# Optimization experiments

Measured on AMD Instinct MI355X. Metric: run time of the kernel, lower is better.

Reference implementation:

```python
import jax, jax.numpy as jnp
import numpy as np

COST_CLASS, COST_MASK, COST_DICE = 2.0, 5.0, 5.0
NUM_POINTS = 12544

def setup_inputs() -> dict:
    key = jax.random.key(0)
    k1, k2, k3, k4, k5 = jax.random.split(key, 5)
    bs, Q, K = 4, 100, 134
    H = W = 256
    M = 80
    P = H * W
    pred_logits = jax.random.normal(k1, (bs, Q, K), dtype=jnp.float32)
    pred_masks = jax.random.normal(k2, (bs, Q, H, W), dtype=jnp.float32)
    tgt_labels = jax.random.randint(k3, (M,), 0, K - 1, dtype=jnp.int32)
    # binary target masks, stored as float (matches .float() in torch code)
    tgt_masks = (jax.random.uniform(k4, (M, H, W)) > 0.5).astype(jnp.float32)
    # random subset of points without replacement (torch.randperm[:num_points])
    point_idx = jax.random.permutation(k5, P)[:NUM_POINTS].astype(jnp.int32)
    return {"pred_logits": pred_logits, "pred_masks": pred_masks,
            "tgt_labels": tgt_labels, "tgt_masks": tgt_masks,
            "point_idx": point_idx}

def reference(pred_logits, pred_masks, tgt_labels, tgt_masks, point_idx):
    bs, Q, K = pred_logits.shape
    N = bs * Q
    M = tgt_masks.shape[0]
    Pn = point_idx.shape[0]

    # class cost: -p[n, tgt_id[m]]
    out_prob = jax.nn.softmax(pred_logits.reshape(N, K), axis=-1)
    tgt_ids = jnp.clip(tgt_labels.astype(jnp.int32), 0, K - 1)
    cost_class = -out_prob[:, tgt_ids]                      # (N, M)

    # sampled mask logits / targets
    x = pred_masks.reshape(N, -1)[:, point_idx]             # (N, Pn) logits
    y = tgt_masks.reshape(M, -1)[:, point_idx]              # (M, Pn) binary float

    # BCE-with-logits cost, separable form:
    # mean_p[softplus(x) - x*y] = mean_p softplus(x) - (x @ y^T)/Pn
    sp_mean = jnp.mean(jax.nn.softplus(x), axis=-1)         # (N,)
    xy = jnp.einsum('np,mp->nm', x, y)                      # (N, M)
    cost_mask = sp_mean[:, None] - xy / Pn

    # dice cost
    s = jax.nn.sigmoid(x)                                   # (N, Pn)
    numer = 2.0 * jnp.einsum('np,mp->nm', s, y)             # (N, M)
    denom = jnp.sum(s, axis=-1)[:, None] + jnp.sum(y, axis=-1)[None, :]
    cost_dice = 1.0 - (numer + 1.0) / (denom + 1.0)

    C = COST_CLASS * cost_class + COST_MASK * cost_mask + COST_DICE * cost_dice
    return C.reshape(bs, Q, M)
```

## Files before the change

### kernel.cpp

```cpp
#include <hip/hip_runtime.h>
#include <math.h>

#define N_ROWS 400
#define M_ROWS 80
#define K_CLS  134
#define PN     12544
#define PFULL  65536
#define WORDS  (PFULL / 32)
#define TSTEPS 392
#define NSUB   25
#define KCG    49
#define TPB    2
#define NM     (N_ROWS * M_ROWS)
#define CHUNK  16384
#define CPB    (PFULL / CHUNK)

typedef __attribute__((ext_vector_type(4))) float  f32x4;
typedef __attribute__((ext_vector_type(8))) __bf16 bf16x8;

__device__ __forceinline__ float wave_reduce_sum(float v) {
#pragma unroll
    for (int off = 32; off > 0; off >>= 1) v += __shfl_down(v, off, 64);
    return v;
}

__global__ __launch_bounds__(1024) void sort_softmax_kernel(
        const int* __restrict__ point_idx,
        unsigned int* __restrict__ bitmap_g, int* __restrict__ rank_g,
        float* __restrict__ rowS_acc, float* __restrict__ rowSP_acc,
        float* __restrict__ ysum_acc,
        const float* __restrict__ pred_logits,
        float* __restrict__ rowmax, float* __restrict__ rowsum) {
    int tid = threadIdx.x;
    if (blockIdx.x == 0) {
        __shared__ unsigned int bits[WORDS];
        __shared__ int wtot[16], wbase[16];
        bits[tid] = 0u; bits[tid + 1024] = 0u;
        if (tid < N_ROWS) { rowS_acc[tid] = 0.f; rowSP_acc[tid] = 0.f; }
        if (tid < M_ROWS) ysum_acc[tid] = 0.f;
        __syncthreads();
        for (int i = tid; i < PN; i += 1024) {
            int p = point_idx[i];
            atomicOr(&bits[p >> 5], 1u << (p & 31));
        }
        __syncthreads();
        unsigned int w0 = bits[tid * 2], w1 = bits[tid * 2 + 1];
        int cnt = __popc(w0) + __popc(w1);
        int lane = tid & 63, wid = tid >> 6;
        int v = cnt;
#pragma unroll
        for (int off = 1; off < 64; off <<= 1) {
            int u = __shfl_up(v, off, 64);
            if (lane >= off) v += u;
        }
        if (lane == 63) wtot[wid] = v;
        __syncthreads();
        if (tid == 0) {
            int run = 0;
#pragma unroll
            for (int i = 0; i < 16; ++i) { wbase[i] = run; run += wtot[i]; }
        }
        __syncthreads();
        int base = wbase[wid] + (v - cnt);
        bitmap_g[tid * 2]     = w0;
        bitmap_g[tid * 2 + 1] = w1;
        rank_g[tid * 2]       = base;
        rank_g[tid * 2 + 1]   = base + __popc(w0);
    } else {
        int wave = tid >> 6, lane = tid & 63;
        int n = (blockIdx.x - 1) * 16 + wave;
        const float* row = pred_logits + n * K_CLS;
        float mx = -1e30f;
        for (int k = lane; k < K_CLS; k += 64) mx = fmaxf(mx, row[k]);
#pragma unroll
        for (int off = 32; off > 0; off >>= 1) mx = fmaxf(mx, __shfl_down(mx, off, 64));
        mx = __shfl(mx, 0, 64);
        float se = 0.f;
        for (int k = lane; k < K_CLS; k += 64) se += expf(row[k] - mx);
        se = wave_reduce_sum(se);
        if (lane == 0) { rowmax[n] = mx; rowsum[n] = se; }
    }
}

__global__ __launch_bounds__(256) void compact_kernel(
        const float* __restrict__ pred_masks, const float* __restrict__ tgt_masks,
        const unsigned int* __restrict__ bitmap_g, const int* __restrict__ rank_g,
        __bf16* __restrict__ Xc, __bf16* __restrict__ Sc, __bf16* __restrict__ Yb,
        float* __restrict__ rowS_acc, float* __restrict__ rowSP_acc,
        float* __restrict__ ysum_acc) {
    __shared__ unsigned int sb[CHUNK / 32];
    __shared__ int swb[CHUNK / 32];
    __shared__ float aS[4], aSP[4];
    int b   = blockIdx.x;
    int row = b / CPB, ch = b % CPB;
    int tid = threadIdx.x;
    int wave = tid >> 6, lane = tid & 63;
    int w0  = ch * (CHUNK / 32);
    sb[tid]        = bitmap_g[w0 + tid];
    sb[tid + 256]  = bitmap_g[w0 + tid + 256];
    swb[tid]       = rank_g[w0 + tid];
    swb[tid + 256] = rank_g[w0 + tid + 256];
    __syncthreads();
    int p0 = ch * CHUNK;

    if (row < N_ROWS) {
        const float* src = pred_masks + (size_t)row * PFULL + p0;
        __bf16* xrow = Xc + (size_t)row * PN;
        __bf16* srow = Sc + (size_t)row * PN;
        float sS = 0.f, sSP = 0.f;
#pragma unroll
        for (int it = 0; it < CHUNK / (256 * 4); ++it) {
            int e = (it * 256 + tid) * 4;
            f32x4 v = *(const f32x4*)(src + e);
            unsigned int w = sb[e >> 5];
            int r = swb[e >> 5] + __popc(w & ((1u << (e & 31)) - 1u));
            unsigned int m4 = (w >> (e & 31)) & 0xFu;
            if (m4) {
#pragma unroll
                for (int k = 0; k < 4; ++k) if (m4 & (1u << k)) {
                    float x  = v[k];
                    float ax = fabsf(x);
                    float ee = __expf(-ax);
                    float den = 1.f + ee;
                    float inv = __builtin_amdgcn_rcpf(den);
                    float sig = (x >= 0.f) ? inv : ee * inv;
                    float sp  = fmaxf(x, 0.f) + __logf(den);
                    xrow[r] = (__bf16)x;
                    srow[r] = (__bf16)sig;
                    sS += sig; sSP += sp; ++r;
                }
            }
        }
        sS  = wave_reduce_sum(sS);
        sSP = wave_reduce_sum(sSP);
        if (lane == 0) { aS[wave] = sS; aSP[wave] = sSP; }
        __syncthreads();
        if (tid == 0)
            atomicAdd(&rowS_acc[row], aS[0] + aS[1] + aS[2] + aS[3]);
        else if (tid == 1)
            atomicAdd(&rowSP_acc[row], aSP[0] + aSP[1] + aSP[2] + aSP[3]);
    } else {
        int m = row - N_ROWS;
        const float* src = tgt_masks + (size_t)m * PFULL + p0;
        int j = m >> 4, colL = m & 15;
        float ys = 0.f;
#pragma unroll
        for (int it = 0; it < CHUNK / (256 * 4); ++it) {
            int e = (it * 256 + tid) * 4;
            f32x4 v = *(const f32x4*)(src + e);
            unsigned int w = sb[e >> 5];
            int r = swb[e >> 5] + __popc(w & ((1u << (e & 31)) - 1u));
            unsigned int m4 = (w >> (e & 31)) & 0xFu;
            if (m4) {
#pragma unroll
                for (int k = 0; k < 4; ++k) if (m4 & (1u << k)) {
                    float y = (v[k] > 0.5f) ? 1.f : 0.f;
                    int t = r >> 5, rr = r & 31;
                    int quad = rr >> 3, jj = rr & 7;
                    Yb[(((size_t)t * 5 + j) * 64 + quad * 16 + colL) * 8 + jj]
                        = (__bf16)y;
                    ys += y; ++r;
                }
            }
        }
        ys = wave_reduce_sum(ys);
        if (lane == 0) aS[wave] = ys;
        __syncthreads();
        if (tid == 0)
            atomicAdd(&ysum_acc[m], aS[0] + aS[1] + aS[2] + aS[3]);
    }
}

__global__ __launch_bounds__(256) void gemm_kernel(
        const __bf16* __restrict__ Xc, const __bf16* __restrict__ Sc,
        const __bf16* __restrict__ Yb,
        float* __restrict__ xypart, float* __restrict__ sypart) {
    __shared__ float red[4][20][64];
    int tid = threadIdx.x;
    int wave = tid >> 6, lane = tid & 63;
    int colL = lane & 15, quad = lane >> 4;
    int nsub = blockIdx.x % NSUB, kcg = blockIdx.x / NSUB;
    int n0 = nsub * 16;
    int tbase = kcg * (TPB * 4) + wave * TPB;
    const bf16x8* Yf = (const bf16x8*)Yb;

    f32x4 accX[5], accS[5];
    f32x4 zero = {0.f, 0.f, 0.f, 0.f};
#pragma unroll
    for (int j = 0; j < 5; ++j) { accX[j] = zero; accS[j] = zero; }

    bf16x8 aX[TPB], aS[TPB], Bb[TPB][5];
#pragma unroll
    for (int i = 0; i < TPB; ++i) {
        int t = tbase + i;
        size_t aoff = (size_t)(n0 + colL) * PN + t * 32 + quad * 8;
        aX[i] = *(const bf16x8*)(Xc + aoff);
        aS[i] = *(const bf16x8*)(Sc + aoff);
        const bf16x8* q = Yf + (size_t)(t * 5) * 64 + lane;
#pragma unroll
        for (int j = 0; j < 5; ++j) Bb[i][j] = q[(size_t)j * 64];
    }
#pragma unroll
    for (int i = 0; i < TPB; ++i) {
#pragma unroll
        for (int j = 0; j < 5; ++j) {
            accX[j] = __builtin_amdgcn_mfma_f32_16x16x32_bf16(aX[i], Bb[i][j], accX[j], 0, 0, 0);
            accS[j] = __builtin_amdgcn_mfma_f32_16x16x32_bf16(aS[i], Bb[i][j], accS[j], 0, 0, 0);
        }
    }

#pragma unroll
    for (int j = 0; j < 5; ++j)
#pragma unroll
        for (int r = 0; r < 4; ++r) red[wave][j * 4 + r][lane] = accX[j][r];
    __syncthreads();
#pragma unroll
    for (int v0 = 0; v0 < 5; ++v0) {
        int v = wave * 5 + v0;
        float s = red[0][v][lane] + red[1][v][lane] + red[2][v][lane] + red[3][v][lane];
        int j = v >> 2, r = v & 3;
        int n = n0 + quad * 4 + r, m = 16 * j + colL;
        xypart[(size_t)kcg * NM + n * M_ROWS + m] = s;
    }
    __syncthreads();
#pragma unroll
    for (int j = 0; j < 5; ++j)
#pragma unroll
        for (int r = 0; r < 4; ++r) red[wave][j * 4 + r][lane] = accS[j][r];
    __syncthreads();
#pragma unroll
    for (int v0 = 0; v0 < 5; ++v0) {
        int v = wave * 5 + v0;
        float s = red[0][v][lane] + red[1][v][lane] + red[2][v][lane] + red[3][v][lane];
        int j = v >> 2, r = v & 3;
        int n = n0 + quad * 4 + r, m = 16 * j + colL;
        sypart[(size_t)kcg * NM + n * M_ROWS + m] = s;
    }
}

__global__ __launch_bounds__(256) void combine_kernel(
        const float* __restrict__ logits,
        const int* __restrict__ tgt_labels,
        const float* __restrict__ rowmax,
        const float* __restrict__ rowsum,
        const float* __restrict__ rowS_acc,
        const float* __restrict__ rowSP_acc,
        const float* __restrict__ ysum_acc,
        const float* __restrict__ xypart,
        const float* __restrict__ sypart,
        float* __restrict__ out) {
    __shared__ float sxy[4][64], ssy[4][64];
    int il = threadIdx.x & 63, q = threadIdx.x >> 6;
    int idx = blockIdx.x * 64 + il;
    int n = idx / M_ROWS, m = idx % M_ROWS;
    float xy = 0.f, sy = 0.f;
    for (int g = q; g < KCG; g += 4) {
        xy += xypart[(size_t)g * NM + idx];
        sy += sypart[(size_t)g * NM + idx];
    }
    sxy[q][il] = xy; ssy[q][il] = sy;
    __syncthreads();
    if (q == 0) {
        xy = sxy[0][il] + sxy[1][il] + sxy[2][il] + sxy[3][il];
        sy = ssy[0][il] + ssy[1][il] + ssy[2][il] + ssy[3][il];
        float ss = rowS_acc[n], sp = rowSP_acc[n], ysum = ysum_acc[m];
        int tc = tgt_labels[m];
        tc = min(max(tc, 0), K_CLS - 1);
        float p = expf(logits[n * K_CLS + tc] - rowmax[n]) / rowsum[n];
        float cost_class = -p;
        float cost_mask = (sp - xy) * (1.0f / PN);
        float cost_dice = 1.f - (2.f * sy + 1.f) / (ss + ysum + 1.f);
        out[idx] = 2.f * cost_class + 5.f * cost_mask + 5.f * cost_dice;
    }
}

extern "C" void kernel_launch(void* const* d_in, const int* in_sizes, int n_in,
                              void* d_out, int out_size, void* d_ws, size_t ws_size,
                              hipStream_t stream) {
    const float* pred_logits = (const float*)d_in[0];
    const float* pred_masks  = (const float*)d_in[1];
    const int*   tgt_labels  = (const int*)d_in[2];
    const float* tgt_masks   = (const float*)d_in[3];
    const int*   point_idx   = (const int*)d_in[4];
    float* out = (float*)d_out;

    char* ws = (char*)d_ws;
    size_t off = 0;
    auto carve = [&](size_t nbytes) {
        char* p = ws + off;
        off += (nbytes + 255) & ~(size_t)255;
        return p;
    };
    unsigned int* bitmap = (unsigned int*)carve(WORDS * 4);
    int*   rankp  = (int*)carve(WORDS * 4);
    float* rowmax = (float*)carve(N_ROWS * 4);
    float* rowsum = (float*)carve(N_ROWS * 4);
    float* rowS_acc  = (float*)carve(N_ROWS * 4);
    float* rowSP_acc = (float*)carve(N_ROWS * 4);
    float* ysum_acc  = (float*)carve(M_ROWS * 4);
    __bf16* Xc = (__bf16*)carve((size_t)N_ROWS * PN * 2);
    __bf16* Sc = (__bf16*)carve((size_t)N_ROWS * PN * 2);
    __bf16* Yb = (__bf16*)carve((size_t)TSTEPS * 5 * 1024);
    float* xypart = (float*)carve((size_t)KCG * NM * 4);
    float* sypart = (float*)carve((size_t)KCG * NM * 4);
    (void)ws_size; (void)in_sizes; (void)n_in; (void)out_size;

    sort_softmax_kernel<<<26, 1024, 0, stream>>>(
        point_idx, bitmap, rankp, rowS_acc, rowSP_acc, ysum_acc,
        pred_logits, rowmax, rowsum);
    compact_kernel<<<(N_ROWS + M_ROWS) * CPB, 256, 0, stream>>>(
        pred_masks, tgt_masks, bitmap, rankp, Xc, Sc, Yb,
        rowS_acc, rowSP_acc, ysum_acc);
    gemm_kernel<<<NSUB * KCG, 256, 0, stream>>>(Xc, Sc, Yb, xypart, sypart);
    combine_kernel<<<NM / 64, 256, 0, stream>>>(
        pred_logits, tgt_labels, rowmax, rowsum, rowS_acc, rowSP_acc,
        ysum_acc, xypart, sypart, out);
}
```

Baseline: 215.3 us.

## Stage compacted points in LDS and write contiguous row-major Y for coalesced stores

The compact kernel now scatters the selected points of each chunk into a shared-memory bf16 buffer first. It then writes them to global memory contiguously, and evaluates sigmoid and softplus only over the compacted points, which spreads the work evenly across threads. The target masks move from a swizzled MFMA-fragment layout to plain row-major Yc, and the GEMM now loads its B fragments from that layout. The chunk size is halved to give more blocks. Softplus and sigmoid are now computed from the bf16-rounded logit instead of the fp32 value, which slightly changes the numerics.

```diff
diff --git a/kernel.cpp b/kernel.cpp
--- a/kernel.cpp
+++ b/kernel.cpp
@@ -12,7 +12,8 @@
 #define KCG    49
 #define TPB    2
 #define NM     (N_ROWS * M_ROWS)
-#define CHUNK  16384
+#define CHUNK  8192
+#define CWORDS (CHUNK / 32)
 #define CPB    (PFULL / CHUNK)
 
 typedef __attribute__((ext_vector_type(4))) float  f32x4;
@@ -85,95 +86,96 @@
 __global__ __launch_bounds__(256) void compact_kernel(
         const float* __restrict__ pred_masks, const float* __restrict__ tgt_masks,
         const unsigned int* __restrict__ bitmap_g, const int* __restrict__ rank_g,
-        __bf16* __restrict__ Xc, __bf16* __restrict__ Sc, __bf16* __restrict__ Yb,
+        __bf16* __restrict__ Xc, __bf16* __restrict__ Sc, __bf16* __restrict__ Yc,
         float* __restrict__ rowS_acc, float* __restrict__ rowSP_acc,
         float* __restrict__ ysum_acc) {
-    __shared__ unsigned int sb[CHUNK / 32];
-    __shared__ int swb[CHUNK / 32];
-    __shared__ float aS[4], aSP[4];
+    __shared__ __bf16 comp[CHUNK];
+    __shared__ unsigned int sb[CWORDS];
+    __shared__ int swb[CWORDS];
+    __shared__ float a0[4], a1[4];
     int b   = blockIdx.x;
     int row = b / CPB, ch = b % CPB;
     int tid = threadIdx.x;
     int wave = tid >> 6, lane = tid & 63;
-    int w0  = ch * (CHUNK / 32);
-    sb[tid]        = bitmap_g[w0 + tid];
-    sb[tid + 256]  = bitmap_g[w0 + tid + 256];
-    swb[tid]       = rank_g[w0 + tid];
-    swb[tid + 256] = rank_g[w0 + tid + 256];
+    int w0  = ch * CWORDS;
+    int gb  = rank_g[w0];
+    int end = (w0 + CWORDS == WORDS) ? PN : rank_g[w0 + CWORDS];
+    int cnt = end - gb;
+    sb[tid]  = bitmap_g[w0 + tid];
+    swb[tid] = rank_g[w0 + tid] - gb;
     __syncthreads();
     int p0 = ch * CHUNK;
-
-    if (row < N_ROWS) {
-        const float* src = pred_masks + (size_t)row * PFULL + p0;
-        __bf16* xrow = Xc + (size_t)row * PN;
-        __bf16* srow = Sc + (size_t)row * PN;
+    bool isX = (row < N_ROWS);
+    const float* src = isX ? (pred_masks + (size_t)row * PFULL + p0)
+                           : (tgt_masks + (size_t)(row - N_ROWS) * PFULL + p0);
+
+#pragma unroll
+    for (int it = 0; it < CHUNK / (256 * 4); ++it) {
+        int e = (it * 256 + tid) * 4;
+        f32x4 v = *(const f32x4*)(src + e);
+        unsigned int w = sb[e >> 5];
+        int bp = e & 31;
+        int r0 = swb[e >> 5] + __popc(w & ((1u << bp) - 1u));
+        unsigned int m4 = (w >> bp) & 0xFu;
+        if (isX) {
+            if (m4 & 1u) comp[r0] = (__bf16)v[0];
+            if (m4 & 2u) comp[r0 + __popc(m4 & 1u)] = (__bf16)v[1];
+            if (m4 & 4u) comp[r0 + __popc(m4 & 3u)] = (__bf16)v[2];
+            if (m4 & 8u) comp[r0 + __popc(m4 & 7u)] = (__bf16)v[3];
+        } else {
+            if (m4 & 1u) comp[r0] = (__bf16)((v[0] > 0.5f) ? 1.f : 0.f);
+            if (m4 & 2u) comp[r0 + __popc(m4 & 1u)] = (__bf16)((v[1] > 0.5f) ? 1.f : 0.f);
+            if (m4 & 4u) comp[r0 + __popc(m4 & 3u)] = (__bf16)((v[2] > 0.5f) ? 1.f : 0.f);
+            if (m4 & 8u) comp[r0 + __popc(m4 & 7u)] = (__bf16)((v[3] > 0.5f) ? 1.f : 0.f);
+        }
+    }
+    __syncthreads();
+
+    if (isX) {
+        __bf16* xrow = Xc + (size_t)row * PN + gb;
+        __bf16* srow = Sc + (size_t)row * PN + gb;
         float sS = 0.f, sSP = 0.f;
-#pragma unroll
-        for (int it = 0; it < CHUNK / (256 * 4); ++it) {
-            int e = (it * 256 + tid) * 4;
-            f32x4 v = *(const f32x4*)(src + e);
-            unsigned int w = sb[e >> 5];
-            int r = swb[e >> 5] + __popc(w & ((1u << (e & 31)) - 1u));
-            unsigned int m4 = (w >> (e & 31)) & 0xFu;
-            if (m4) {
-#pragma unroll
-                for (int k = 0; k < 4; ++k) if (m4 & (1u << k)) {
-                    float x  = v[k];
-                    float ax = fabsf(x);
-                    float ee = __expf(-ax);
-                    float den = 1.f + ee;
-                    float inv = __builtin_amdgcn_rcpf(den);
-                    float sig = (x >= 0.f) ? inv : ee * inv;
-                    float sp  = fmaxf(x, 0.f) + __logf(den);
-                    xrow[r] = (__bf16)x;
-                    srow[r] = (__bf16)sig;
-                    sS += sig; sSP += sp; ++r;
-                }
-            }
+        for (int i = tid; i < cnt; i += 256) {
+            __bf16 xb = comp[i];
+            float x  = (float)xb;
+            float ax = fabsf(x);
+            float ee = __expf(-ax);
+            float den = 1.f + ee;
+            float inv = __builtin_amdgcn_rcpf(den);
+            float sig = (x >= 0.f) ? inv : ee * inv;
+            float sp  = fmaxf(x, 0.f) + __logf(den);
+            xrow[i] = xb;
+            srow[i] = (__bf16)sig;
+            sS += sig; sSP += sp;
         }
         sS  = wave_reduce_sum(sS);
         sSP = wave_reduce_sum(sSP);
-        if (lane == 0) { aS[wave] = sS; aSP[wave] = sSP; }
+        if (lane == 0) { a0[wave] = sS; a1[wave] = sSP; }
         __syncthreads();
         if (tid == 0)
-            atomicAdd(&rowS_acc[row], aS[0] + aS[1] + aS[2] + aS[3]);
+            atomicAdd(&rowS_acc[row], a0[0] + a0[1] + a0[2] + a0[3]);
         else if (tid == 1)
-            atomicAdd(&rowSP_acc[row], aSP[0] + aSP[1] + aSP[2] + aSP[3]);
+            atomicAdd(&rowSP_acc[row], a1[0] + a1[1] + a1[2] + a1[3]);
     } else {
         int m = row - N_ROWS;
-        const float* src = tgt_masks + (size_t)m * PFULL + p0;
-        int j = m >> 4, colL = m & 15;
+        __bf16* yrow = Yc + (size_t)m * PN + gb;
         float ys = 0.f;
-#pragma unroll
-        for (int it = 0; it < CHUNK / (256 * 4); ++it) {
-            int e = (it * 256 + tid) * 4;
-            f32x4 v = *(const f32x4*)(src + e);
-            unsigned int w = sb[e >> 5];
-            int r = swb[e >> 5] + __popc(w & ((1u << (e & 31)) - 1u));
-            unsigned int m4 = (w >> (e & 31)) & 0xFu;
-            if (m4) {
-#pragma unroll
-                for (int k = 0; k < 4; ++k) if (m4 & (1u << k)) {
-                    float y = (v[k] > 0.5f) ? 1.f : 0.f;
-                    int t = r >> 5, rr = r & 31;
-                    int quad = rr >> 3, jj = rr & 7;
-                    Yb[(((size_t)t * 5 + j) * 64 + quad * 16 + colL) * 8 + jj]
-                        = (__bf16)y;
-                    ys += y; ++r;
-                }
-            }
+        for (int i = tid; i < cnt; i += 256) {
+            __bf16 y = comp[i];
+            yrow[i] = y;
+            ys += (float)y;
         }
         ys = wave_reduce_sum(ys);
-        if (lane == 0) aS[wave] = ys;
+        if (lane == 0) a0[wave] = ys;
         __syncthreads();
         if (tid == 0)
-            atomicAdd(&ysum_acc[m], aS[0] + aS[1] + aS[2] + aS[3]);
+            atomicAdd(&ysum_acc[m], a0[0] + a0[1] + a0[2] + a0[3]);
     }
 }
 
 __global__ __launch_bounds__(256) void gemm_kernel(
         const __bf16* __restrict__ Xc, const __bf16* __restrict__ Sc,
-        const __bf16* __restrict__ Yb,
+        const __bf16* __restrict__ Yc,
         float* __restrict__ xypart, float* __restrict__ sypart) {
     __shared__ float red[4][20][64];
     int tid = threadIdx.x;
@@ -182,7 +184,6 @@
     int nsub = blockIdx.x % NSUB, kcg = blockIdx.x / NSUB;
     int n0 = nsub * 16;
     int tbase = kcg * (TPB * 4) + wave * TPB;
-    const bf16x8* Yf = (const bf16x8*)Yb;
 
     f32x4 accX[5], accS[5];
     f32x4 zero = {0.f, 0.f, 0.f, 0.f};
@@ -193,12 +194,13 @@
 #pragma unroll
     for (int i = 0; i < TPB; ++i) {
         int t = tbase + i;
-        size_t aoff = (size_t)(n0 + colL) * PN + t * 32 + quad * 8;
+        int k0 = t * 32 + quad * 8;
+        size_t aoff = (size_t)(n0 + colL) * PN + k0;
         aX[i] = *(const bf16x8*)(Xc + aoff);
         aS[i] = *(const bf16x8*)(Sc + aoff);
-        const bf16x8* q = Yf + (size_t)(t * 5) * 64 + lane;
-#pragma unroll
-        for (int j = 0; j < 5; ++j) Bb[i][j] = q[(size_t)j * 64];
+#pragma unroll
+        for (int j = 0; j < 5; ++j)
+            Bb[i][j] = *(const bf16x8*)(Yc + (size_t)(16 * j + colL) * PN + k0);
     }
 #pragma unroll
     for (int i = 0; i < TPB; ++i) {
@@ -300,7 +302,7 @@
     float* ysum_acc  = (float*)carve(M_ROWS * 4);
     __bf16* Xc = (__bf16*)carve((size_t)N_ROWS * PN * 2);
     __bf16* Sc = (__bf16*)carve((size_t)N_ROWS * PN * 2);
-    __bf16* Yb = (__bf16*)carve((size_t)TSTEPS * 5 * 1024);
+    __bf16* Yc = (__bf16*)carve((size_t)M_ROWS * PN * 2);
     float* xypart = (float*)carve((size_t)KCG * NM * 4);
     float* sypart = (float*)carve((size_t)KCG * NM * 4);
     (void)ws_size; (void)in_sizes; (void)n_in; (void)out_size;
@@ -309,9 +311,9 @@
         point_idx, bitmap, rankp, rowS_acc, rowSP_acc, ysum_acc,
         pred_logits, rowmax, rowsum);
     compact_kernel<<<(N_ROWS + M_ROWS) * CPB, 256, 0, stream>>>(
-        pred_masks, tgt_masks, bitmap, rankp, Xc, Sc, Yb,
+        pred_masks, tgt_masks, bitmap, rankp, Xc, Sc, Yc,
         rowS_acc, rowSP_acc, ysum_acc);
-    gemm_kernel<<<NSUB * KCG, 256, 0, stream>>>(Xc, Sc, Yb, xypart, sypart);
+    gemm_kernel<<<NSUB * KCG, 256, 0, stream>>>(Xc, Sc, Yc, xypart, sypart);
     combine_kernel<<<NM / 64, 256, 0, stream>>>(
         pred_logits, tgt_labels, rowmax, rowsum, rowS_acc, rowSP_acc,
         ysum_acc, xypart, sypart, out);
```

After: 208.7 us. -3.1%, faster.
